# Kernel tuning notes

Hardware: AMD Instinct MI355X
Metric: run time of the kernel (lower is better)

## Reference

```python
import jax, jax.numpy as jnp
import numpy as np

B, S, H, E, V, L = 64, 400, 512, 300, 50000, 1


def setup_inputs() -> dict:
    key = jax.random.key(0)
    ks = jax.random.split(key, 16)
    s = lambda k, shape, fan: jax.random.normal(k, shape, jnp.float32) * (1.0 / np.sqrt(fan))
    return {
        "x": jax.random.randint(ks[0], (B,), 0, V),
        "enc_out": jax.random.normal(ks[1], (B, S, H), jnp.float32),
        "h0": jax.random.normal(ks[2], (L, B, H), jnp.float32),
        "c0": jax.random.normal(ks[3], (L, B, H), jnp.float32),
        "text": jax.random.randint(ks[4], (B, S), 0, V),
        "batch_size": B,
        "emb_table": jax.random.normal(ks[5], (V, E), jnp.float32),
        "V_w": s(ks[6], (1, H), H),
        "V_b": jnp.zeros((1,), jnp.float32),
        "gen_w": s(ks[7], (1, 2 * H + E), 2 * H + E),
        "gen_b": jnp.zeros((1,), jnp.float32),
        "out_w": s(ks[8], (V, 2 * H), 2 * H),
        "out_b": jnp.zeros((V,), jnp.float32),
        "W_ih": s(ks[9], (4 * H, E + H), E + H),
        "W_hh": s(ks[10], (4 * H, H), H),
        "b_ih": jnp.zeros((4 * H,), jnp.float32),
        "b_hh": jnp.zeros((4 * H,), jnp.float32),
    }


def reference(x, enc_out, h0, c0, text, batch_size, emb_table, V_w, V_b,
              gen_w, gen_b, out_w, out_b, W_ih, W_hh, b_ih, b_hh):
    xe = emb_table[x]                                   # [B,E] (dropout off in eval)
    h_prev, c_prev = h0[0], c0[0]                       # [B,H], layers==1
    # Bahdanau attention: V(tanh(enc_out + dec_h)) softmaxed over seq
    score = jnp.tanh(enc_out + h_prev[:, None, :]) @ V_w.T + V_b   # [B,S,1]
    enc_weight = jax.nn.softmax(score, axis=1)                      # [B,S,1]
    ctx = jnp.sum(enc_weight * enc_out, axis=1)                     # [B,H]
    # single-step LSTM cell (torch gate order: i,f,g,o)
    d_in = jnp.concatenate([xe, ctx], axis=-1)                      # [B,E+H]
    gates = d_in @ W_ih.T + h_prev @ W_hh.T + b_ih + b_hh           # [B,4H]
    i, f, g, o = jnp.split(gates, 4, axis=-1)
    c_new = jax.nn.sigmoid(f) * c_prev + jax.nn.sigmoid(i) * jnp.tanh(g)
    h_new = jax.nn.sigmoid(o) * jnp.tanh(c_new)                     # [B,H]
    # pointer-generator combine
    out_cat = jnp.concatenate([h_new, ctx], axis=-1)                # [B,2H]
    gen_in = jnp.concatenate([ctx, h_new, xe], axis=-1)             # [B,2H+E]
    p_gen = jax.nn.sigmoid(gen_in @ gen_w.T + gen_b)[:, 0]          # [B]
    p_ptr = 1.0 - p_gen
    rows = jnp.arange(batch_size)[:, None]                          # [B,1]
    ptr_prob = jnp.zeros((batch_size, out_w.shape[0]), enc_out.dtype)
    ptr_prob = ptr_prob.at[rows, text].set(enc_weight[:, :, 0])     # scatter-set
    gen_prob = out_cat @ out_w.T + out_b                            # [B,V]
    out_prob = p_ptr[:, None] * ptr_prob + p_gen[:, None] * gen_prob
    return out_prob, h_new[None], c_new[None]
```

## Files before the change

### kernel.cpp

```cpp
#include <hip/hip_runtime.h>
#include <hip/hip_bf16.h>

#define BB 64
#define SS 400
#define HH 512
#define EE 300
#define VV 50000
#define KD 812
#define KG 1324
#define KC 1024
#define BV (BB*VV)

typedef __attribute__((ext_vector_type(8))) short bf16x8;
typedef __attribute__((ext_vector_type(4))) float f32x4;

#define WS_SCORE 0
#define WS_ML    25600
#define WS_MLB   26624
#define WS_CTX   51200
#define WS_HNEW  83968
#define WS_G0    116736
#define WS_G1    247808
#define WS_G2    378880
#define WS_G3    509952
#define WS_PGEN  641024
#define WS_PART  641088
#define WS_ABF   903232
#define WS_AD1   936000
#define WS_AD2   962624

__device__ __forceinline__ float sigm(float x){ return 1.f/(1.f+__expf(-x)); }
__device__ __forceinline__ float ftanh(float x){
  x = fminf(fmaxf(x,-15.f),15.f);
  float e = __expf(2.f*x);
  return (e-1.f)/(e+1.f);
}
__device__ __forceinline__ unsigned short f2bf(float f){
  unsigned int u = __builtin_bit_cast(unsigned int, f);
  u += 0x7fffu + ((u>>16)&1u);
  return (unsigned short)(u>>16);
}

#define LDW(S, off) { w##S##0 = *(const float4*)(wr + (off)*32); \
                      w##S##1 = *(const float4*)(wr + (off)*32 + 4); }
#define LDA(S, off) { a##S##0 = *(const bf16x8*)(a0 + (off)*32); \
                      a##S##1 = *(const bf16x8*)(a1 + (off)*32); \
                      a##S##2 = *(const bf16x8*)(a2 + (off)*32); \
                      a##S##3 = *(const bf16x8*)(a3 + (off)*32); }
#define CONS(S) { union { bf16x8 v; unsigned int u[4]; } bb_; \
  float4 f0_ = w##S##0; float4 f1_ = w##S##1; \
  asm("v_cvt_pk_bf16_f32 %0, %1, %2" : "=v"(bb_.u[0]) : "v"(f0_.x), "v"(f0_.y)); \
  asm("v_cvt_pk_bf16_f32 %0, %1, %2" : "=v"(bb_.u[1]) : "v"(f0_.z), "v"(f0_.w)); \
  asm("v_cvt_pk_bf16_f32 %0, %1, %2" : "=v"(bb_.u[2]) : "v"(f1_.x), "v"(f1_.y)); \
  asm("v_cvt_pk_bf16_f32 %0, %1, %2" : "=v"(bb_.u[3]) : "v"(f1_.z), "v"(f1_.w)); \
  acc0 = __builtin_amdgcn_mfma_f32_16x16x32_bf16(a##S##0, bb_.v, acc0, 0,0,0); \
  acc1 = __builtin_amdgcn_mfma_f32_16x16x32_bf16(a##S##1, bb_.v, acc1, 0,0,0); \
  acc2 = __builtin_amdgcn_mfma_f32_16x16x32_bf16(a##S##2, bb_.v, acc2, 0,0,0); \
  acc3 = __builtin_amdgcn_mfma_f32_16x16x32_bf16(a##S##3, bb_.v, acc3, 0,0,0); }

template<int NSTEP>
__device__ __forceinline__ void mfma_seg2(const float* __restrict__ wr,
    const unsigned short* __restrict__ a0, const unsigned short* __restrict__ a1,
    const unsigned short* __restrict__ a2, const unsigned short* __restrict__ a3,
    f32x4& acc0, f32x4& acc1, f32x4& acc2, f32x4& acc3)
{
  static_assert(NSTEP % 2 == 0 && NSTEP >= 4, "");
  float4 wA0,wA1, wB0,wB1;
  bf16x8 aA0,aA1,aA2,aA3, aB0,aB1,aB2,aB3;
  LDW(A,0) LDA(A,0)
  LDW(B,1) LDA(B,1)
  #pragma unroll
  for (int ks=0; ks<NSTEP; ks+=2){
    CONS(A) if (ks+2 < NSTEP){ LDW(A,ks+2) LDA(A,ks+2) }
    CONS(B) if (ks+3 < NSTEP){ LDW(B,ks+3) LDA(B,ks+3) }
  }
}

__global__ __launch_bounds__(256) void k_prep(const int* __restrict__ x,
    const float* __restrict__ emb, const float* __restrict__ h0,
    unsigned short* __restrict__ ad1, unsigned short* __restrict__ ad2)
{
  int n = blockIdx.x*256 + threadIdx.x;
  if (n < BB*832){
    int b = n/832, k = n - b*832;
    if (k < EE) ad1[n] = f2bf(emb[(size_t)x[b]*EE + k]);
    else if (k >= 812) ad1[n] = 0;
  } else {
    int m = n - BB*832;
    ad2[m] = f2bf(h0[m]);
  }
}

__global__ __launch_bounds__(256) void k_scorectx(const float* __restrict__ enc,
    const float* __restrict__ h0, const float* __restrict__ Vw,
    const float* __restrict__ Vb, float* __restrict__ score,
    float* __restrict__ part, float* __restrict__ ml)
{
  __shared__ float wl[52];
  __shared__ float we[52];
  int b = blockIdx.x >> 3, sp = blockIdx.x & 7;
  int t = threadIdx.x, w = t >> 6, lane = t & 63;
  int i0 = lane*8;
  const float4* hp = (const float4*)(h0 + b*HH + i0);
  const float4* vp = (const float4*)(Vw + i0);
  float4 hv0 = hp[0], hv1 = hp[1];
  float4 v0 = vp[0], v1 = vp[1];
  float vb = Vb[0];
  for (int r = w; r < 50; r += 4){
    int s = sp*50 + r;
    const float4* ep = (const float4*)(enc + ((size_t)b*SS + s)*HH + i0);
    float4 e0 = ep[0], e1 = ep[1];
    float sum = ftanh(e0.x+hv0.x)*v0.x + ftanh(e0.y+hv0.y)*v0.y
              + ftanh(e0.z+hv0.z)*v0.z + ftanh(e0.w+hv0.w)*v0.w
              + ftanh(e1.x+hv1.x)*v1.x + ftanh(e1.y+hv1.y)*v1.y
              + ftanh(e1.z+hv1.z)*v1.z + ftanh(e1.w+hv1.w)*v1.w;
    #pragma unroll
    for (int off=32; off; off>>=1) sum += __shfl_xor(sum, off);
    if (lane==0){ float sc = sum + vb; wl[r] = sc; score[b*SS + s] = sc; }
  }
  __syncthreads();
  float mx = -1e30f;
  for (int s=0; s<50; ++s) mx = fmaxf(mx, wl[s]);
  if (t < 50) we[t] = __expf(wl[t] - mx);
  __syncthreads();
  float l = 0.f;
  for (int s=0; s<50; ++s) l += we[s];
  float a0 = 0.f, a1 = 0.f;
  const float* ebase = enc + ((size_t)b*SS + sp*50)*HH + 2*t;
  #pragma unroll 5
  for (int s=0; s<50; ++s){
    float wg = we[s];
    float2 e = *(const float2*)(ebase + s*HH);
    a0 += wg * e.x;
    a1 += wg * e.y;
  }
  *(float2*)(part + (size_t)(b*8+sp)*HH + 2*t) = make_float2(a0, a1);
  if (t == 0){ ml[(b*8+sp)*2] = mx; ml[(b*8+sp)*2+1] = l; }
}

__global__ __launch_bounds__(256) void k_ctx_reduce(const float* __restrict__ part,
    const float* __restrict__ ml, float* __restrict__ ctx,
    unsigned short* __restrict__ ad1, float* __restrict__ mlb)
{
  int b = blockIdx.x, t = threadIdx.x;
  float M = -1e30f;
  #pragma unroll
  for (int c=0; c<8; ++c) M = fmaxf(M, ml[(b*8+c)*2]);
  float L = 0.f, sc[8];
  #pragma unroll
  for (int c=0; c<8; ++c){
    sc[c] = __expf(ml[(b*8+c)*2] - M);
    L += ml[(b*8+c)*2+1] * sc[c];
  }
  float inv = 1.f / L;
  float a0=0.f, a1=0.f;
  #pragma unroll
  for (int c=0; c<8; ++c){
    float2 e = *(const float2*)(part + (size_t)(b*8+c)*HH + 2*t);
    a0 += sc[c]*e.x; a1 += sc[c]*e.y;
  }
  a0 *= inv; a1 *= inv;
  *(float2*)(ctx + b*HH + 2*t) = make_float2(a0, a1);
  ad1[b*832 + EE + 2*t]     = f2bf(a0);
  ad1[b*832 + EE + 2*t + 1] = f2bf(a1);
  if (t == 0){ mlb[b*2] = M; mlb[b*2+1] = L; }
}

__global__ __launch_bounds__(128, 4) void k_gates(const float* __restrict__ Wih,
    const float* __restrict__ Whh, const unsigned short* __restrict__ ad1,
    const unsigned short* __restrict__ ad2,
    float* __restrict__ g0, float* __restrict__ g1,
    float* __restrict__ g2, float* __restrict__ g3)
{
  int wt = blockIdx.x*2 + (threadIdx.x >> 6);
  int lane = threadIdx.x & 63;
  int col = lane & 15, kg = lane >> 4;
  int jt = wt >> 2, part = wt & 3;
  int j = jt*16 + col;
  f32x4 acc0={0.f,0.f,0.f,0.f}, acc1=acc0, acc2=acc0, acc3=acc0;
  float* g;
  if (part < 2){
    int k0 = part ? 384 : 0;
    const float* wr = Wih + (size_t)j*KD + k0 + kg*8;
    const unsigned short* a = ad1 + col*832 + k0 + kg*8;
    if (part) mfma_seg2<14>(wr, a, a+16*832, a+32*832, a+48*832, acc0,acc1,acc2,acc3);
    else      mfma_seg2<12>(wr, a, a+16*832, a+32*832, a+48*832, acc0,acc1,acc2,acc3);
    g = part ? g1 : g0;
  } else {
    int k0 = (part==3) ? 256 : 0;
    const float* wr = Whh + (size_t)j*HH + k0 + kg*8;
    const unsigned short* a = ad2 + col*512 + k0 + kg*8;
    mfma_seg2<8>(wr, a, a+16*512, a+32*512, a+48*512, acc0,acc1,acc2,acc3);
    g = (part==3) ? g3 : g2;
  }
  #pragma unroll
  for (int i=0;i<4;i++){
    g[(size_t)j*BB + 0*16 + kg*4 + i] = acc0[i];
    g[(size_t)j*BB + 1*16 + kg*4 + i] = acc1[i];
    g[(size_t)j*BB + 2*16 + kg*4 + i] = acc2[i];
    g[(size_t)j*BB + 3*16 + kg*4 + i] = acc3[i];
  }
}

__global__ __launch_bounds__(256) void k_lstm(const float* __restrict__ c0,
    const float* __restrict__ bih, const float* __restrict__ bhh,
    const float* __restrict__ g0, const float* __restrict__ g1,
    const float* __restrict__ g2, const float* __restrict__ g3,
    const float* __restrict__ ctx, float* __restrict__ hnew,
    unsigned short* __restrict__ abf, float* __restrict__ out)
{
  int n = blockIdx.x*256 + threadIdx.x;
  int b = n & 63, h = n >> 6;
  #define GSUM(off) (g0[(off)*BB+b] + g1[(off)*BB+b] + g2[(off)*BB+b] + g3[(off)*BB+b] + bih[off] + bhh[off])
  float gi = GSUM(h);
  float gf = GSUM(HH+h);
  float gg = GSUM(2*HH+h);
  float go = GSUM(3*HH+h);
  #undef GSUM
  float cn = sigm(gf)*c0[b*HH+h] + sigm(gi)*ftanh(gg);
  float hn = sigm(go)*ftanh(cn);
  out[BV + b*HH + h]          = hn;
  out[BV + BB*HH + b*HH + h]  = cn;
  hnew[b*HH + h] = hn;
  abf[b*KC + h]      = f2bf(hn);
  abf[b*KC + HH + h] = f2bf(ctx[b*HH + h]);
}

__global__ __launch_bounds__(256) void k_pgen(const float* __restrict__ genw,
    const float* __restrict__ genb, const float* __restrict__ ctx,
    const float* __restrict__ hnew, const int* __restrict__ x,
    const float* __restrict__ emb, float* __restrict__ pgen)
{
  __shared__ float red[256];
  int b = blockIdx.x, t = threadIdx.x;
  float p = 0.f;
  for (int k=t; k<KG; k+=256){
    float g = genw[k];
    float v = (k < HH) ? ctx[b*HH + k]
            : (k < 2*HH) ? hnew[b*HH + k - HH]
            : emb[(size_t)x[b]*EE + (k - 2*HH)];
    p += g*v;
  }
  red[t] = p; __syncthreads();
  for (int o=128; o; o>>=1){ if (t<o) red[t] += red[t+o]; __syncthreads(); }
  if (t==0) pgen[b] = sigm(red[0] + genb[0]);
}

#define QPAD 1040
__global__ __launch_bounds__(256, 2) void k_gemm(const float* __restrict__ out_w,
    const float* __restrict__ out_b, const unsigned short* __restrict__ abf,
    const float* __restrict__ pgen, float* __restrict__ out)
{
  __shared__ __align__(16) char wlds[2][16*QPAD];
  int t = threadIdx.x, w = t >> 6, lane = t & 63;
  int col = lane & 15, kg = lane >> 4;
  int bid = blockIdx.x;
  int ts = (bid * 3125) >> 9;
  int te = ((bid + 1) * 3125) >> 9;
  int NS = (te - ts) * 4;

  const unsigned short* ap = abf + (size_t)(w*16 + col)*KC + kg*8;
  bf16x8 pa[32];
  #pragma unroll
  for (int k=0; k<32; ++k) pa[k] = *(const bf16x8*)(ap + k*32);

  float4 st0, st1, st2, st3;
  #define LOADSTEP(h_) { \
    int tile_ = ts + ((h_) >> 2), q_ = (h_) & 3; \
    const char* gp_ = (const char*)out_w + (size_t)tile_*65536 + (w*4)*4096 + q_*1024 + lane*16; \
    st0 = *(const float4*)(gp_); \
    st1 = *(const float4*)(gp_ + 4096); \
    st2 = *(const float4*)(gp_ + 8192); \
    st3 = *(const float4*)(gp_ + 12288); }
  #define WRITESTEP(buf_) { \
    char* lp_ = &wlds[buf_][0] + (w*4)*QPAD + lane*16; \
    *(float4*)(lp_)          = st0; \
    *(float4*)(lp_ + QPAD)   = st1; \
    *(float4*)(lp_ + 2*QPAD) = st2; \
    *(float4*)(lp_ + 3*QPAD) = st3; }
  #define RAWBAR() { asm volatile("" ::: "memory"); \
    __builtin_amdgcn_s_barrier(); \
    asm volatile("" ::: "memory"); }
  #define QCOMP(QL) { \
    const char* rb_ = &wlds[h & 1][0] + col*QPAD + kg*32; \
    _Pragma("unroll") \
    for (int ks=0; ks<8; ++ks){ \
      float4 f0 = *(const float4*)(rb_ + ks*128); \
      float4 f1 = *(const float4*)(rb_ + ks*128 + 16); \
      union { bf16x8 v; unsigned int u[4]; } bb; \
      asm("v_cvt_pk_bf16_f32 %0, %1, %2" : "=v"(bb.u[0]) : "v"(f0.x), "v"(f0.y)); \
      asm("v_cvt_pk_bf16_f32 %0, %1, %2" : "=v"(bb.u[1]) : "v"(f0.z), "v"(f0.w)); \
      asm("v_cvt_pk_bf16_f32 %0, %1, %2" : "=v"(bb.u[2]) : "v"(f1.x), "v"(f1.y)); \
      asm("v_cvt_pk_bf16_f32 %0, %1, %2" : "=v"(bb.u[3]) : "v"(f1.z), "v"(f1.w)); \
      acc = __builtin_amdgcn_mfma_f32_16x16x32_bf16(pa[(QL)*8+ks], bb.v, acc, 0,0,0); \
    } }

  LOADSTEP(0)
  asm volatile("s_waitcnt vmcnt(0)" ::: "memory");
  __builtin_amdgcn_sched_barrier(0);
  WRITESTEP(0)
  asm volatile("s_waitcnt lgkmcnt(0)" ::: "memory");
  RAWBAR();

  f32x4 acc = {0.f,0.f,0.f,0.f};
  for (int h = 0; h < NS; ++h){
    int q = h & 3;
    if (h + 1 < NS) LOADSTEP(h+1)

    if      (q == 0){ QCOMP(0) }
    else if (q == 1){ QCOMP(1) }
    else if (q == 2){ QCOMP(2) }
    else            { QCOMP(3) }

    if (h + 1 < NS){
      asm volatile("s_waitcnt vmcnt(0)" ::: "memory");
      __builtin_amdgcn_sched_barrier(0);
      WRITESTEP((h+1) & 1)
      asm volatile("s_waitcnt lgkmcnt(0)" ::: "memory");
    }
    if (q == 3){
      int tile = ts + (h >> 2);
      int v = tile*16 + col;
      float ob = out_b[v];
      #pragma unroll
      for (int i=0;i<4;i++){
        int b = w*16 + kg*4 + i;
        out[(size_t)b*VV + v] = pgen[b]*(acc[i] + ob);
      }
      acc = (f32x4){0.f,0.f,0.f,0.f};
    }
    RAWBAR();
  }
  #undef LOADSTEP
  #undef WRITESTEP
  #undef RAWBAR
  #undef QCOMP
}

__global__ __launch_bounds__(256) void k_scatter(const int* __restrict__ text,
    const float* __restrict__ score, const float* __restrict__ mlb,
    const float* __restrict__ pgen, float* __restrict__ out)
{
  __shared__ int ts[SS];
  int b = blockIdx.x, t = threadIdx.x;
  ts[t] = text[b*SS + t];
  if (t + 256 < SS) ts[t+256] = text[b*SS + t + 256];
  __syncthreads();
  float pp = 1.f - pgen[b];
  float M = mlb[b*2], invL = 1.f / mlb[b*2+1];
  #pragma unroll
  for (int rep=0; rep<2; ++rep){
    int s = t + rep*256;
    if (s < SS){
      int v = ts[s];
      bool dup = false;
      #pragma unroll 4
      for (int s2=s+1; s2<SS; ++s2) dup = dup || (ts[s2]==v);
      if (!dup){
        float wgt = __expf(score[b*SS + s] - M) * invL;
        out[(size_t)b*VV + v] += pp * wgt;
      }
    }
  }
}

extern "C" void kernel_launch(void* const* d_in, const int* in_sizes, int n_in,
                              void* d_out, int out_size, void* d_ws, size_t ws_size,
                              hipStream_t stream)
{
  const int*   x    = (const int*)  d_in[0];
  const float* enc  = (const float*)d_in[1];
  const float* h0   = (const float*)d_in[2];
  const float* c0   = (const float*)d_in[3];
  const int*   text = (const int*)  d_in[4];
  const float* emb  = (const float*)d_in[6];
  const float* Vw   = (const float*)d_in[7];
  const float* Vb   = (const float*)d_in[8];
  const float* genw = (const float*)d_in[9];
  const float* genb = (const float*)d_in[10];
  const float* outw = (const float*)d_in[11];
  const float* outb = (const float*)d_in[12];
  const float* Wih  = (const float*)d_in[13];
  const float* Whh  = (const float*)d_in[14];
  const float* bih  = (const float*)d_in[15];
  const float* bhh  = (const float*)d_in[16];
  float* out = (float*)d_out;

  float* ws     = (float*)d_ws;
  float* score  = ws + WS_SCORE;
  float* ml     = ws + WS_ML;
  float* mlb    = ws + WS_MLB;
  float* ctx    = ws + WS_CTX;
  float* hnew   = ws + WS_HNEW;
  float* g0     = ws + WS_G0;
  float* g1     = ws + WS_G1;
  float* g2     = ws + WS_G2;
  float* g3     = ws + WS_G3;
  float* pgen   = ws + WS_PGEN;
  float* part   = ws + WS_PART;
  unsigned short* abf = (unsigned short*)(ws + WS_ABF);
  unsigned short* ad1 = (unsigned short*)(ws + WS_AD1);
  unsigned short* ad2 = (unsigned short*)(ws + WS_AD2);

  k_prep<<<336, 256, 0, stream>>>(x, emb, h0, ad1, ad2);
  k_scorectx<<<512, 256, 0, stream>>>(enc, h0, Vw, Vb, score, part, ml);
  k_ctx_reduce<<<64, 256, 0, stream>>>(part, ml, ctx, ad1, mlb);
  k_gates<<<256, 128, 0, stream>>>(Wih, Whh, ad1, ad2, g0, g1, g2, g3);
  k_lstm<<<128, 256, 0, stream>>>(c0, bih, bhh, g0, g1, g2, g3, ctx, hnew, abf, out);
  k_pgen<<<64, 256, 0, stream>>>(genw, genb, ctx, hnew, x, emb, pgen);
  k_gemm<<<512, 256, 0, stream>>>(outw, outb, abf, pgen, out);
  k_scatter<<<64, 256, 0, stream>>>(text, score, mlb, pgen, out);
}
```

Before: 126.5 us.

## Convert out_w tiles to bf16 before LDS staging with swizzled layout and half-K steps

The vocab-projection GEMM now loads each weight tile in two half-K steps of 8 nontemporal float4 loads per thread. It converts to bf16 before writing to a 16x1024-byte XOR-swizzled LDS buffer rather than a padded fp32 one. MFMA operands then read directly as bf16x8 with no per-step conversion, which halves LDS traffic and removes bank-conflict padding. The loop now uses one __syncthreads per step with the next global load issued after the barrier, dropping the explicit waitcnt/sched_barrier choreography. The trade-off is more registers in flight per thread and a less tightly controlled load-to-write overlap.

Result: slower. 138.4 us (+9.4%).

```diff
diff --git a/kernel.cpp b/kernel.cpp
--- a/kernel.cpp
+++ b/kernel.cpp
@@ -13,6 +13,7 @@
 
 typedef __attribute__((ext_vector_type(8))) short bf16x8;
 typedef __attribute__((ext_vector_type(4))) float f32x4;
+typedef __attribute__((ext_vector_type(4))) unsigned int u32x4;
 
 #define WS_SCORE 0
 #define WS_ML    25600
@@ -246,80 +247,78 @@
   if (t==0) pgen[b] = sigm(red[0] + genb[0]);
 }
 
-#define QPAD 1040
 __global__ __launch_bounds__(256, 2) void k_gemm(const float* __restrict__ out_w,
     const float* __restrict__ out_b, const unsigned short* __restrict__ abf,
     const float* __restrict__ pgen, float* __restrict__ out)
 {
-  __shared__ __align__(16) char wlds[2][16*QPAD];
+  __shared__ __align__(16) char wlds[2][16*1024];
   int t = threadIdx.x, w = t >> 6, lane = t & 63;
   int col = lane & 15, kg = lane >> 4;
+  int row = t >> 4;
+  int jc  = t & 15;
   int bid = blockIdx.x;
   int ts = (bid * 3125) >> 9;
   int te = ((bid + 1) * 3125) >> 9;
-  int NS = (te - ts) * 4;
+  int NS = (te - ts) * 2;
 
   const unsigned short* ap = abf + (size_t)(w*16 + col)*KC + kg*8;
   bf16x8 pa[32];
   #pragma unroll
   for (int k=0; k<32; ++k) pa[k] = *(const bf16x8*)(ap + k*32);
 
-  float4 st0, st1, st2, st3;
-  #define LOADSTEP(h_) { \
-    int tile_ = ts + ((h_) >> 2), q_ = (h_) & 3; \
-    const char* gp_ = (const char*)out_w + (size_t)tile_*65536 + (w*4)*4096 + q_*1024 + lane*16; \
-    st0 = *(const float4*)(gp_); \
-    st1 = *(const float4*)(gp_ + 4096); \
-    st2 = *(const float4*)(gp_ + 8192); \
-    st3 = *(const float4*)(gp_ + 12288); }
-  #define WRITESTEP(buf_) { \
-    char* lp_ = &wlds[buf_][0] + (w*4)*QPAD + lane*16; \
-    *(float4*)(lp_)          = st0; \
-    *(float4*)(lp_ + QPAD)   = st1; \
-    *(float4*)(lp_ + 2*QPAD) = st2; \
-    *(float4*)(lp_ + 3*QPAD) = st3; }
-  #define RAWBAR() { asm volatile("" ::: "memory"); \
-    __builtin_amdgcn_s_barrier(); \
-    asm volatile("" ::: "memory"); }
-  #define QCOMP(QL) { \
-    const char* rb_ = &wlds[h & 1][0] + col*QPAD + kg*32; \
+  f32x4 s0,s1,s2,s3,s4,s5,s6,s7;
+
+  #define LOADH(h_) { \
+    int tile_ = ts + ((h_) >> 1), kh_ = (h_) & 1; \
+    const char* gp_ = (const char*)out_w + (size_t)tile_*65536 + row*4096 + kh_*2048 + jc*32; \
+    s0 = __builtin_nontemporal_load((const f32x4*)(gp_)); \
+    s1 = __builtin_nontemporal_load((const f32x4*)(gp_ + 16)); \
+    s2 = __builtin_nontemporal_load((const f32x4*)(gp_ + 512)); \
+    s3 = __builtin_nontemporal_load((const f32x4*)(gp_ + 528)); \
+    s4 = __builtin_nontemporal_load((const f32x4*)(gp_ + 1024)); \
+    s5 = __builtin_nontemporal_load((const f32x4*)(gp_ + 1040)); \
+    s6 = __builtin_nontemporal_load((const f32x4*)(gp_ + 1536)); \
+    s7 = __builtin_nontemporal_load((const f32x4*)(gp_ + 1552)); }
+
+  #define CVT16(d_, a_, b_) { \
+    asm("v_cvt_pk_bf16_f32 %0, %1, %2" : "=v"(d_.x) : "v"(a_.x), "v"(a_.y)); \
+    asm("v_cvt_pk_bf16_f32 %0, %1, %2" : "=v"(d_.y) : "v"(a_.z), "v"(a_.w)); \
+    asm("v_cvt_pk_bf16_f32 %0, %1, %2" : "=v"(d_.z) : "v"(b_.x), "v"(b_.y)); \
+    asm("v_cvt_pk_bf16_f32 %0, %1, %2" : "=v"(d_.w) : "v"(b_.z), "v"(b_.w)); }
+
+  #define WRITEH(buf_) { \
+    char* lb_ = &wlds[buf_][0] + row*1024; \
+    int sw_ = (row & 7) << 4; \
+    u32x4 q0, q1, q2, q3; \
+    CVT16(q0, s0, s1) CVT16(q1, s2, s3) CVT16(q2, s4, s5) CVT16(q3, s6, s7) \
+    *(u32x4*)(lb_ + ((jc*16      ) ^ sw_)) = q0; \
+    *(u32x4*)(lb_ + ((jc*16 + 256) ^ sw_)) = q1; \
+    *(u32x4*)(lb_ + ((jc*16 + 512) ^ sw_)) = q2; \
+    *(u32x4*)(lb_ + ((jc*16 + 768) ^ sw_)) = q3; }
+
+  #define COMPH(buf_, PB_) { \
+    const char* rb_ = &wlds[buf_][0] + col*1024; \
+    int swr_ = (col & 7) << 4; \
     _Pragma("unroll") \
-    for (int ks=0; ks<8; ++ks){ \
-      float4 f0 = *(const float4*)(rb_ + ks*128); \
-      float4 f1 = *(const float4*)(rb_ + ks*128 + 16); \
-      union { bf16x8 v; unsigned int u[4]; } bb; \
-      asm("v_cvt_pk_bf16_f32 %0, %1, %2" : "=v"(bb.u[0]) : "v"(f0.x), "v"(f0.y)); \
-      asm("v_cvt_pk_bf16_f32 %0, %1, %2" : "=v"(bb.u[1]) : "v"(f0.z), "v"(f0.w)); \
-      asm("v_cvt_pk_bf16_f32 %0, %1, %2" : "=v"(bb.u[2]) : "v"(f1.x), "v"(f1.y)); \
-      asm("v_cvt_pk_bf16_f32 %0, %1, %2" : "=v"(bb.u[3]) : "v"(f1.z), "v"(f1.w)); \
-      acc = __builtin_amdgcn_mfma_f32_16x16x32_bf16(pa[(QL)*8+ks], bb.v, acc, 0,0,0); \
+    for (int ks=0; ks<16; ++ks){ \
+      bf16x8 bfr = *(const bf16x8*)(rb_ + ((ks*64 + kg*16) ^ swr_)); \
+      acc = __builtin_amdgcn_mfma_f32_16x16x32_bf16(pa[(PB_)+ks], bfr, acc, 0,0,0); \
     } }
 
-  LOADSTEP(0)
-  asm volatile("s_waitcnt vmcnt(0)" ::: "memory");
-  __builtin_amdgcn_sched_barrier(0);
-  WRITESTEP(0)
-  asm volatile("s_waitcnt lgkmcnt(0)" ::: "memory");
-  RAWBAR();
-
+  LOADH(0)
   f32x4 acc = {0.f,0.f,0.f,0.f};
   for (int h = 0; h < NS; ++h){
-    int q = h & 3;
-    if (h + 1 < NS) LOADSTEP(h+1)
-
-    if      (q == 0){ QCOMP(0) }
-    else if (q == 1){ QCOMP(1) }
-    else if (q == 2){ QCOMP(2) }
-    else            { QCOMP(3) }
-
-    if (h + 1 < NS){
-      asm volatile("s_waitcnt vmcnt(0)" ::: "memory");
-      __builtin_amdgcn_sched_barrier(0);
-      WRITESTEP((h+1) & 1)
-      asm volatile("s_waitcnt lgkmcnt(0)" ::: "memory");
-    }
-    if (q == 3){
-      int tile = ts + (h >> 2);
+    if ((h & 1) == 0){
+      WRITEH(0)
+      __syncthreads();
+      if (h + 1 < NS) LOADH(h+1)
+      COMPH(0, 0)
+    } else {
+      WRITEH(1)
+      __syncthreads();
+      if (h + 1 < NS) LOADH(h+1)
+      COMPH(1, 16)
+      int tile = ts + (h >> 1);
       int v = tile*16 + col;
       float ob = out_b[v];
       #pragma unroll
@@ -329,12 +328,11 @@
       }
       acc = (f32x4){0.f,0.f,0.f,0.f};
     }
-    RAWBAR();
-  }
-  #undef LOADSTEP
-  #undef WRITESTEP
-  #undef RAWBAR
-  #undef QCOMP
+  }
+  #undef LOADH
+  #undef CVT16
+  #undef WRITEH
+  #undef COMPH
 }
 
 __global__ __launch_bounds__(256) void k_scatter(const int* __restrict__ text,
```

## Fuse prep into score kernel and deepen output GEMM load pipeline

Applied to the files above, without the earlier changes.

The separate prep kernel, which converts embeddings and h0 to bf16, is folded into k_scorectx as 336 extra blocks, removing one launch. The output-projection GEMM is restructured to stage half a tile (2048 bytes of K) per LDS step with two register staging sets. Global loads are issued through inline asm and waited on with partial vmcnt counts, so weight loads for the next tile stay in flight while the current tile computes. This raises register use (two staging sets plus the A fragments) and relies on exact vmcnt accounting, which is fragile if the number of issued loads changes.

After: 118.1 us. 6.7% less time.

```diff
diff --git a/kernel.cpp b/kernel.cpp
--- a/kernel.cpp
+++ b/kernel.cpp
@@ -76,28 +76,27 @@
   }
 }
 
-__global__ __launch_bounds__(256) void k_prep(const int* __restrict__ x,
-    const float* __restrict__ emb, const float* __restrict__ h0,
-    unsigned short* __restrict__ ad1, unsigned short* __restrict__ ad2)
-{
-  int n = blockIdx.x*256 + threadIdx.x;
-  if (n < BB*832){
-    int b = n/832, k = n - b*832;
-    if (k < EE) ad1[n] = f2bf(emb[(size_t)x[b]*EE + k]);
-    else if (k >= 812) ad1[n] = 0;
-  } else {
-    int m = n - BB*832;
-    ad2[m] = f2bf(h0[m]);
-  }
-}
-
-__global__ __launch_bounds__(256) void k_scorectx(const float* __restrict__ enc,
+__global__ __launch_bounds__(256) void k_scorectx(const int* __restrict__ x,
+    const float* __restrict__ emb, const float* __restrict__ enc,
     const float* __restrict__ h0, const float* __restrict__ Vw,
     const float* __restrict__ Vb, float* __restrict__ score,
-    float* __restrict__ part, float* __restrict__ ml)
+    float* __restrict__ part, float* __restrict__ ml,
+    unsigned short* __restrict__ ad1, unsigned short* __restrict__ ad2)
 {
   __shared__ float wl[52];
   __shared__ float we[52];
+  if (blockIdx.x >= 512){
+    int n = (blockIdx.x - 512)*256 + threadIdx.x;
+    if (n < BB*832){
+      int b = n/832, k = n - b*832;
+      if (k < EE) ad1[n] = f2bf(emb[(size_t)x[b]*EE + k]);
+      else if (k >= 812) ad1[n] = 0;
+    } else {
+      int m = n - BB*832;
+      ad2[m] = f2bf(h0[m]);
+    }
+    return;
+  }
   int b = blockIdx.x >> 3, sp = blockIdx.x & 7;
   int t = threadIdx.x, w = t >> 6, lane = t & 63;
   int i0 = lane*8;
@@ -246,45 +245,72 @@
   if (t==0) pgen[b] = sigm(red[0] + genb[0]);
 }
 
-#define QPAD 1040
+#define PADH 2064
+#define GLDX4(dst, ptr) asm volatile("global_load_dwordx4 %0, %1, off" : "=v"(dst) : "v"(ptr));
+#define GLD1(dst, ptr)  asm volatile("global_load_dword %0, %1, off"   : "=v"(dst) : "v"(ptr));
+#define WAITV(N) { asm volatile("s_waitcnt vmcnt(" #N ")" ::: "memory"); \
+                   __builtin_amdgcn_sched_barrier(0); }
+#define BARR() { asm volatile("s_waitcnt lgkmcnt(0)" ::: "memory"); \
+                 __builtin_amdgcn_sched_barrier(0); \
+                 __builtin_amdgcn_s_barrier(); \
+                 __builtin_amdgcn_sched_barrier(0); }
+
 __global__ __launch_bounds__(256, 2) void k_gemm(const float* __restrict__ out_w,
     const float* __restrict__ out_b, const unsigned short* __restrict__ abf,
     const float* __restrict__ pgen, float* __restrict__ out)
 {
-  __shared__ __align__(16) char wlds[2][16*QPAD];
+  __shared__ __align__(16) char wlds[2][16*PADH];
   int t = threadIdx.x, w = t >> 6, lane = t & 63;
   int col = lane & 15, kg = lane >> 4;
   int bid = blockIdx.x;
   int ts = (bid * 3125) >> 9;
   int te = ((bid + 1) * 3125) >> 9;
-  int NS = (te - ts) * 4;
-
+
+  int gtb = ((t >> 7) << 12) + ((t & 127) << 4);
+  int ltb = (t >> 7) * PADH + ((t & 127) << 4);
+
+  bf16x8 pa0[16], pa1[16];
   const unsigned short* ap = abf + (size_t)(w*16 + col)*KC + kg*8;
-  bf16x8 pa[32];
-  #pragma unroll
-  for (int k=0; k<32; ++k) pa[k] = *(const bf16x8*)(ap + k*32);
-
-  float4 st0, st1, st2, st3;
-  #define LOADSTEP(h_) { \
-    int tile_ = ts + ((h_) >> 2), q_ = (h_) & 3; \
-    const char* gp_ = (const char*)out_w + (size_t)tile_*65536 + (w*4)*4096 + q_*1024 + lane*16; \
-    st0 = *(const float4*)(gp_); \
-    st1 = *(const float4*)(gp_ + 4096); \
-    st2 = *(const float4*)(gp_ + 8192); \
-    st3 = *(const float4*)(gp_ + 12288); }
-  #define WRITESTEP(buf_) { \
-    char* lp_ = &wlds[buf_][0] + (w*4)*QPAD + lane*16; \
-    *(float4*)(lp_)          = st0; \
-    *(float4*)(lp_ + QPAD)   = st1; \
-    *(float4*)(lp_ + 2*QPAD) = st2; \
-    *(float4*)(lp_ + 3*QPAD) = st3; }
-  #define RAWBAR() { asm volatile("" ::: "memory"); \
-    __builtin_amdgcn_s_barrier(); \
-    asm volatile("" ::: "memory"); }
-  #define QCOMP(QL) { \
-    const char* rb_ = &wlds[h & 1][0] + col*QPAD + kg*32; \
+  #pragma unroll
+  for (int k=0; k<16; ++k){ GLDX4(pa0[k], (ap + k*32)) }
+  #pragma unroll
+  for (int k=0; k<16; ++k){ GLDX4(pa1[k], (ap + 512 + k*32)) }
+  float pg0, pg1, pg2, pg3;
+  {
+    const float* pb = pgen + w*16 + kg*4;
+    GLD1(pg0, (pb)) GLD1(pg1, (pb+1)) GLD1(pg2, (pb+2)) GLD1(pg3, (pb+3))
+  }
+
+  f32x4 sA_0,sA_1,sA_2,sA_3,sA_4,sA_5,sA_6,sA_7;
+  f32x4 sB_0,sB_1,sB_2,sB_3,sB_4,sB_5,sB_6,sB_7;
+  float obA, obB;
+
+  #define WLOAD(S, tile_, kh_) { \
+    const char* gp_ = (const char*)out_w + (size_t)(tile_)*65536 + (kh_)*2048 + gtb; \
+    GLDX4(s##S##_0, (gp_)) \
+    GLDX4(s##S##_1, (gp_ + 8192)) \
+    GLDX4(s##S##_2, (gp_ + 16384)) \
+    GLDX4(s##S##_3, (gp_ + 24576)) \
+    GLDX4(s##S##_4, (gp_ + 32768)) \
+    GLDX4(s##S##_5, (gp_ + 40960)) \
+    GLDX4(s##S##_6, (gp_ + 49152)) \
+    GLDX4(s##S##_7, (gp_ + 57344)) }
+
+  #define WSTORE(S, buf_) { \
+    char* lp_ = &wlds[buf_][0] + ltb; \
+    *(f32x4*)(lp_)            = s##S##_0; \
+    *(f32x4*)(lp_ + 2*PADH)   = s##S##_1; \
+    *(f32x4*)(lp_ + 4*PADH)   = s##S##_2; \
+    *(f32x4*)(lp_ + 6*PADH)   = s##S##_3; \
+    *(f32x4*)(lp_ + 8*PADH)   = s##S##_4; \
+    *(f32x4*)(lp_ + 10*PADH)  = s##S##_5; \
+    *(f32x4*)(lp_ + 12*PADH)  = s##S##_6; \
+    *(f32x4*)(lp_ + 14*PADH)  = s##S##_7; }
+
+  #define COMPH(buf_, PA_) { \
+    const char* rb_ = &wlds[buf_][0] + col*PADH + kg*32; \
     _Pragma("unroll") \
-    for (int ks=0; ks<8; ++ks){ \
+    for (int ks=0; ks<16; ++ks){ \
       float4 f0 = *(const float4*)(rb_ + ks*128); \
       float4 f1 = *(const float4*)(rb_ + ks*128 + 16); \
       union { bf16x8 v; unsigned int u[4]; } bb; \
@@ -292,49 +318,43 @@
       asm("v_cvt_pk_bf16_f32 %0, %1, %2" : "=v"(bb.u[1]) : "v"(f0.z), "v"(f0.w)); \
       asm("v_cvt_pk_bf16_f32 %0, %1, %2" : "=v"(bb.u[2]) : "v"(f1.x), "v"(f1.y)); \
       asm("v_cvt_pk_bf16_f32 %0, %1, %2" : "=v"(bb.u[3]) : "v"(f1.z), "v"(f1.w)); \
-      acc = __builtin_amdgcn_mfma_f32_16x16x32_bf16(pa[(QL)*8+ks], bb.v, acc, 0,0,0); \
+      acc = __builtin_amdgcn_mfma_f32_16x16x32_bf16(PA_[ks], bb.v, acc, 0,0,0); \
     } }
 
-  LOADSTEP(0)
-  asm volatile("s_waitcnt vmcnt(0)" ::: "memory");
-  __builtin_amdgcn_sched_barrier(0);
-  WRITESTEP(0)
-  asm volatile("s_waitcnt lgkmcnt(0)" ::: "memory");
-  RAWBAR();
+  WLOAD(A, ts, 0)
+  GLD1(obA, (out_b + ts*16 + col))
+  WLOAD(B, ts, 1)
 
   f32x4 acc = {0.f,0.f,0.f,0.f};
-  for (int h = 0; h < NS; ++h){
-    int q = h & 3;
-    if (h + 1 < NS) LOADSTEP(h+1)
-
-    if      (q == 0){ QCOMP(0) }
-    else if (q == 1){ QCOMP(1) }
-    else if (q == 2){ QCOMP(2) }
-    else            { QCOMP(3) }
-
-    if (h + 1 < NS){
-      asm volatile("s_waitcnt vmcnt(0)" ::: "memory");
-      __builtin_amdgcn_sched_barrier(0);
-      WRITESTEP((h+1) & 1)
-      asm volatile("s_waitcnt lgkmcnt(0)" ::: "memory");
+  #pragma unroll 1
+  for (int tile = ts; tile < te; ++tile){
+    WAITV(9)
+    WSTORE(A, 0)
+    if (tile + 1 < te){
+      WLOAD(A, tile+1, 0)
+      GLD1(obB, (out_b + (tile+1)*16 + col))
     }
-    if (q == 3){
-      int tile = ts + (h >> 2);
+    BARR()
+    COMPH(0, pa0)
+    if (tile + 1 < te){ WAITV(9) } else { WAITV(0) }
+    WSTORE(B, 1)
+    if (tile + 1 < te) WLOAD(B, tile+1, 1)
+    BARR()
+    COMPH(1, pa1)
+    {
       int v = tile*16 + col;
-      float ob = out_b[v];
-      #pragma unroll
-      for (int i=0;i<4;i++){
-        int b = w*16 + kg*4 + i;
-        out[(size_t)b*VV + v] = pgen[b]*(acc[i] + ob);
-      }
-      acc = (f32x4){0.f,0.f,0.f,0.f};
+      int b0 = w*16 + kg*4;
+      out[(size_t)(b0+0)*VV + v] = pg0*(acc[0] + obA);
+      out[(size_t)(b0+1)*VV + v] = pg1*(acc[1] + obA);
+      out[(size_t)(b0+2)*VV + v] = pg2*(acc[2] + obA);
+      out[(size_t)(b0+3)*VV + v] = pg3*(acc[3] + obA);
     }
-    RAWBAR();
-  }
-  #undef LOADSTEP
-  #undef WRITESTEP
-  #undef RAWBAR
-  #undef QCOMP
+    acc = (f32x4){0.f,0.f,0.f,0.f};
+    obA = obB;
+  }
+  #undef WLOAD
+  #undef WSTORE
+  #undef COMPH
 }
 
 __global__ __launch_bounds__(256) void k_scatter(const int* __restrict__ text,
@@ -402,8 +422,7 @@
   unsigned short* ad1 = (unsigned short*)(ws + WS_AD1);
   unsigned short* ad2 = (unsigned short*)(ws + WS_AD2);
 
-  k_prep<<<336, 256, 0, stream>>>(x, emb, h0, ad1, ad2);
-  k_scorectx<<<512, 256, 0, stream>>>(enc, h0, Vw, Vb, score, part, ml);
+  k_scorectx<<<848, 256, 0, stream>>>(x, emb, enc, h0, Vw, Vb, score, part, ml, ad1, ad2);
   k_ctx_reduce<<<64, 256, 0, stream>>>(part, ml, ctx, ad1, mlb);
   k_gates<<<256, 128, 0, stream>>>(Wih, Whh, ad1, ad2, g0, g1, g2, g3);
   k_lstm<<<128, 256, 0, stream>>>(c0, bih, bhh, g0, g1, g2, g3, ctx, hnew, abf, out);
```
